# Optimization experiments

Hardware: AMD Instinct MI355X
Metric: run time of the kernel (lower is better)

## Reference

```python
import jax, jax.numpy as jnp
import numpy as np

N, CIN, COUT = 8, 256, 512
HEADS, DK, DV = 8, 256, 256
MAP = 32          # H = W = map_size
KS, PAD = 3, 1
DKH = DK // HEADS  # 32
DVH = DV // HEADS  # 32
CONV_OUT = COUT - DV  # 256


def conv2d(x, w, b, stride=1, padding=0):
    out = jax.lax.conv_general_dilated(
        x, w, (stride, stride), [(padding, padding), (padding, padding)],
        dimension_numbers=("NCHW", "OIHW", "NCHW"))
    return out + b[None, :, None, None]


def rel_to_abs(x):
    # x: [B, G, L, 2L-1] relative logits -> [B, G, L, L] absolute (skewing trick)
    B, G, L, _ = x.shape
    x = jnp.pad(x, ((0, 0), (0, 0), (0, 0), (0, 1)))          # [B,G,L,2L]
    flat = x.reshape(B, G, L * 2 * L)
    flat = jnp.pad(flat, ((0, 0), (0, 0), (0, L - 1)))
    return flat.reshape(B, G, L + 1, 2 * L - 1)[:, :, :L, L - 1:]


def setup_inputs() -> dict:
    key = jax.random.key(0)
    ks = jax.random.split(key, 16)
    def w(k, shape, fan_in):
        return jax.random.normal(k, shape, jnp.float32) * (fan_in ** -0.5)
    inp = {
        "x": jax.random.normal(ks[0], (N, CIN, MAP, MAP), jnp.float32),
        "conv_w": w(ks[1], (CONV_OUT, CIN, KS, KS), CIN * KS * KS),
        "conv_b": jnp.zeros((CONV_OUT,), jnp.float32),
        "q_w": w(ks[2], (DK, CIN, KS, KS), CIN * KS * KS),
        "q_b": jnp.zeros((DK,), jnp.float32),
        "k_w": w(ks[3], (DK, CIN, KS, KS), CIN * KS * KS),
        "k_b": jnp.zeros((DK,), jnp.float32),
        "v_w": w(ks[4], (DV, CIN, KS, KS), CIN * KS * KS),
        "v_b": jnp.zeros((DV,), jnp.float32),
        "attn_w": w(ks[5], (DV, DV, 1, 1), DV),
        "attn_b": jnp.zeros((DV,), jnp.float32),
        "width_mat": jax.random.normal(ks[6], (2 * MAP - 1, DKH), jnp.float32) * (DKH ** -0.5),
        "height_mat": jax.random.normal(ks[7], (2 * MAP - 1, DKH), jnp.float32) * (DKH ** -0.5),
    }
    return inp


def reference(x, conv_w, conv_b, q_w, q_b, k_w, k_b, v_w, v_b,
              attn_w, attn_b, width_mat, height_mat):
    conv_maps = conv2d(x, conv_w, conv_b, 1, PAD)            # [N, 256, H, W]
    H = W = MAP
    q = conv2d(x, q_w, q_b, 1, PAD).reshape(N, HEADS, DKH, H, W)
    k = conv2d(x, k_w, k_b, 1, PAD).reshape(N, HEADS, DKH, H, W)
    v = conv2d(x, v_w, v_b, 1, PAD).reshape(N, HEADS, DVH, H, W)

    qf = q.reshape(N, HEADS, DKH, H * W)
    kf = k.reshape(N, HEADS, DKH, H * W)
    vf = v.reshape(N, HEADS, DVH, H * W)
    logits = jnp.einsum("nhdq,nhdk->nhqk", qf, kf)           # [N,h,HW,HW]

    qp = q.transpose(0, 1, 3, 4, 2)                          # [N,h,H,W,dkh]
    # width relative logits: depends on (hq, wq, wk), broadcast over hk
    rel_w = jnp.einsum("nhyxd,rd->nhyxr", qp, width_mat)     # [N,h,H,W,2W-1]
    abs_w = rel_to_abs(rel_w.reshape(N, HEADS * H, W, 2 * W - 1)
                       ).reshape(N, HEADS, H, W, W)          # [N,h,hq,wq,wk]
    # height relative logits: depends on (wq, hq, hk), broadcast over wk
    rel_h = jnp.einsum("nhyxd,rd->nhxyr", qp, height_mat)    # [N,h,W,H,2H-1]
    abs_h = rel_to_abs(rel_h.reshape(N, HEADS * W, H, 2 * H - 1)
                       ).reshape(N, HEADS, W, H, H)          # [N,h,wq,hq,hk]

    w_bias = abs_w[:, :, :, :, None, :]                      # [N,h,hq,wq,1,wk]
    h_bias = abs_h.transpose(0, 1, 3, 2, 4)[..., None]       # [N,h,hq,wq,hk,1]
    logits = (logits.reshape(N, HEADS, H, W, H, W) + h_bias + w_bias
              ).reshape(N, HEADS, H * W, H * W)
    logits = logits * (DKH ** -0.5)

    weights = jax.nn.softmax(logits, axis=-1)
    attn = jnp.einsum("nhqk,nhdk->nhqd", weights, vf)        # [N,h,HW,dvh]
    # faithful to torch .view quirk: row-major reshape [HW,dvh] -> [dvh,H,W]
    attn_maps = attn.reshape(N, HEADS * DVH, H, W)
    attn_maps = conv2d(attn_maps, attn_w, attn_b, 1, 0)
    return jnp.concatenate([conv_maps, attn_maps], axis=1)
```

## Files before the change

### kernel.cpp

```cpp
#include <hip/hip_runtime.h>
#include <hip/hip_bf16.h>


typedef __attribute__((ext_vector_type(8))) __bf16 bf16x8;
typedef __attribute__((ext_vector_type(4))) float f32x4;
typedef unsigned short u16;
typedef unsigned int u32;
typedef __attribute__((ext_vector_type(8))) u16 u16x8;

#define GLD(gp, lp) __builtin_amdgcn_global_load_lds( \
    (const __attribute__((address_space(1))) u32*)(gp), \
    (__attribute__((address_space(3))) u32*)(lp), 16, 0, 0)

static __device__ __forceinline__ u16 f2bf(float f) {
  u32 u = __builtin_bit_cast(u32, f);
  u += 0x7fffu + ((u >> 16) & 1u);
  return (u16)(u >> 16);
}
static __device__ __forceinline__ float bf2f(u16 h) {
  return __builtin_bit_cast(float, (u32)h << 16);
}

__global__ __launch_bounds__(256) void k_cast_w(
    const float* __restrict__ conv_w, const float* __restrict__ q_w,
    const float* __restrict__ k_w, const float* __restrict__ v_w,
    const float* __restrict__ attn_w, u16* __restrict__ W9, u16* __restrict__ W1) {
  __shared__ float t[2304];
  int row = blockIdx.x;
  const float* src = row < 256 ? conv_w : row < 512 ? q_w : row < 768 ? k_w : v_w;
  const float* sr = src + (row & 255) * 2304;
#pragma unroll
  for (int i = threadIdx.x; i < 2304; i += 256) t[i] = sr[i];
  __syncthreads();
  u16* dr = W9 + row * 2304;
#pragma unroll
  for (int i = threadIdx.x; i < 2304; i += 256) {
    int t9 = i >> 8, c = i & 255;
    dr[i] = f2bf(t[c * 9 + t9]);
  }
  if (row < 256) W1[row * 256 + threadIdx.x] = f2bf(attn_w[row * 256 + threadIdx.x]);
}

__global__ void k_xT(const float* __restrict__ x, u16* __restrict__ xT,
                     u16* __restrict__ zpage) {
  if (blockIdx.x == 0 && threadIdx.x < 512) zpage[threadIdx.x] = 0;
  __shared__ float t[32][33];
  int b = blockIdx.x;
  int sb = b & 31, cb = (b >> 5) & 7, n = b >> 8;
  int s0 = sb << 5, c0 = cb << 5;
  int ls = threadIdx.x & 31, lc = threadIdx.x >> 5;
#pragma unroll
  for (int i = 0; i < 4; ++i) {
    int c = lc + i * 8;
    t[c][ls] = x[(((n << 8) + c0 + c) << 10) + s0 + ls];
  }
  __syncthreads();
#pragma unroll
  for (int i = 0; i < 4; ++i) {
    int s = lc + i * 8;
    xT[(((n << 10) + s0 + s) << 8) + c0 + ls] = f2bf(t[ls][s]);
  }
}

__global__ __launch_bounds__(512) void k_gemm_conv(
    const u16* __restrict__ A, const u16* __restrict__ xT, const u16* __restrict__ zpage,
    float* __restrict__ out,
    u16* __restrict__ qb, u16* __restrict__ kb, u16* __restrict__ vb,
    const float* __restrict__ conv_b, const float* __restrict__ q_b,
    const float* __restrict__ k_b, const float* __restrict__ v_b) {
  __shared__ u16 As[8192], Bs[8192];
  f32x4 acc[4][2] = {};
  const int tid = threadIdx.x;
  const int wave = tid >> 6, lane = tid & 63;
  const int wr = wave >> 2, wc = wave & 3;
  const int lr = lane & 15, lk = lane >> 4;
  const int srow = lane >> 3;
  const int scol = (lane & 7) << 3;
  const int bm = blockIdx.x, bn = blockIdx.y;

  int bn_y[2], bn_x[2], bn_base[2];
#pragma unroll
  for (int i = 0; i < 2; ++i) {
    int seg = i * 8 + wave;
    int col = bn * 128 + seg * 8 + srow;
    int n = col >> 10, s = col & 1023;
    bn_y[i] = s >> 5;
    bn_x[i] = s & 31;
    bn_base[i] = n << 10;
  }

  for (int k0 = 0; k0 < 2304; k0 += 64) {
    int t9 = k0 >> 8;
    int dy = t9 / 3 - 1, dx = t9 - (t9 / 3) * 3 - 1;
    int c0 = k0 & 255;
#pragma unroll
    for (int i = 0; i < 2; ++i) {
      int seg = i * 8 + wave;
      GLD(A + (bm * 128 + seg * 8 + srow) * 2304 + k0 + scol, As + seg * 512);
      int sy = bn_y[i] + dy, sx = bn_x[i] + dx;
      bool ok = ((u32)sy < 32u) && ((u32)sx < 32u);
      const u16* src = ok ? (xT + ((bn_base[i] + (sy << 5) + sx) << 8) + c0 + scol)
                          : (zpage + scol);
      GLD(src, Bs + seg * 512);
    }
    __syncthreads();
#pragma unroll
    for (int kk = 0; kk < 2; ++kk) {
      bf16x8 af[4], bv[2];
#pragma unroll
      for (int m = 0; m < 4; ++m)
        af[m] = *(const bf16x8*)&As[(wr * 64 + m * 16 + lr) * 64 + kk * 32 + lk * 8];
#pragma unroll
      for (int n = 0; n < 2; ++n)
        bv[n] = *(const bf16x8*)&Bs[(wc * 32 + n * 16 + lr) * 64 + kk * 32 + lk * 8];
#pragma unroll
      for (int m = 0; m < 4; ++m)
#pragma unroll
        for (int n = 0; n < 2; ++n)
          acc[m][n] = __builtin_amdgcn_mfma_f32_16x16x32_bf16(af[m], bv[n], acc[m][n], 0, 0, 0);
    }
    __syncthreads();
  }

  const int row0 = bm * 128 + wr * 64 + lk * 4;
  const int col0 = bn * 128 + wc * 32 + lr;
#pragma unroll
  for (int m = 0; m < 4; ++m) {
#pragma unroll
    for (int n = 0; n < 2; ++n) {
      int col = col0 + n * 16;
      int nn = col >> 10, s = col & 1023;
#pragma unroll
      for (int j = 0; j < 4; ++j) {
        int c = row0 + m * 16 + j;
        float v = acc[m][n][j];
        if (c < 256) {
          out[((nn << 9) + c) * 1024 + s] = v + conv_b[c];
        } else if (c < 512) {
          int cc = c - 256;
          qb[((((nn << 3) + (cc >> 5)) << 10) + s) * 32 + (cc & 31)] = f2bf(v + q_b[cc]);
        } else if (c < 768) {
          int cc = c - 512;
          kb[((((nn << 3) + (cc >> 5)) << 10) + s) * 32 + (cc & 31)] = f2bf(v + k_b[cc]);
        } else {
          int cc = c - 768;
          vb[((nn << 8) + cc) * 1024 + s] = f2bf(v + v_b[cc]);
        }
      }
    }
  }
}

__global__ __launch_bounds__(256) void k_bias(const u16* __restrict__ qb,
                                              const float* __restrict__ wm,
                                              const float* __restrict__ hm,
                                              float* __restrict__ Bw, float* __restrict__ Bh) {
  int pos = blockIdx.x * blockDim.x + threadIdx.x;
  int s = pos & 1023;
  int y = s >> 5, xx = s & 31;
  float q[32];
  const u16x8* q8 = (const u16x8*)(qb + pos * 32);
#pragma unroll
  for (int v = 0; v < 4; ++v) {
    u16x8 w = q8[v];
#pragma unroll
    for (int e = 0; e < 8; ++e) q[v * 8 + e] = bf2f(w[e]);
  }
  float* bwo = Bw + pos * 32;
  float* bho = Bh + pos * 32;
#pragma unroll 4
  for (int r = 0; r < 32; ++r) {
    const f32x4* wr = (const f32x4*)(wm + (r - xx + 31) * 32);
    const f32x4* hr = (const f32x4*)(hm + (r - y + 31) * 32);
    float aw = 0.f, ah = 0.f;
#pragma unroll
    for (int i = 0; i < 8; ++i) {
      f32x4 wv = wr[i], hv = hr[i];
#pragma unroll
      for (int e = 0; e < 4; ++e) {
        float qd = q[i * 4 + e];
        aw += qd * wv[e];
        ah += qd * hv[e];
      }
    }
    bwo[r] = aw;
    bho[r] = ah;
  }
}

__global__ __launch_bounds__(256) void k_attn(
    const u16* __restrict__ qb, const u16* __restrict__ kb, const u16* __restrict__ vb,
    const float* __restrict__ Bw, const float* __restrict__ Bh, u16* __restrict__ AMT) {
  __shared__ u16 Pl[4][1024];
  const int wave = threadIdx.x >> 6, lane = threadIdx.x & 63;
  const int task = blockIdx.x * 4 + wave;
  const int nh = task >> 6, qg = task & 63;
  const int n = nh >> 3, h = nh & 7;
  const int qbase = qg << 4;
  const int lr = lane & 15, lg = lane >> 4;

  bf16x8 aq = *(const bf16x8*)&qb[((nh << 10) + qbase + lr) * 32 + lg * 8];

  float Bwr[2][4];
#pragma unroll
  for (int p = 0; p < 2; ++p)
#pragma unroll
    for (int j = 0; j < 4; ++j)
      Bwr[p][j] = Bw[((nh << 10) + qbase + lg * 4 + j) * 32 + p * 16 + lr];

  float mrow[4] = {-1e30f, -1e30f, -1e30f, -1e30f};
  float lrow[4] = {0.f, 0.f, 0.f, 0.f};
  f32x4 o[2] = {};
  u16* pl = Pl[wave];

  for (int kt = 0; kt < 16; ++kt) {
    f32x4 zero = {0.f, 0.f, 0.f, 0.f};
    f32x4 sf_[4];
#pragma unroll
    for (int f = 0; f < 4; ++f) {
      bf16x8 bk = *(const bf16x8*)&kb[((nh << 10) + (kt << 6) + f * 16 + lr) * 32 + lg * 8];
      sf_[f] = __builtin_amdgcn_mfma_f32_16x16x32_bf16(aq, bk, zero, 0, 0, 0);
    }
    float Bhr[2][4];
#pragma unroll
    for (int p = 0; p < 2; ++p)
#pragma unroll
      for (int j = 0; j < 4; ++j)
        Bhr[p][j] = Bh[((nh << 10) + qbase + lg * 4 + j) * 32 + (kt << 1) + p];
    float tv[4][4];
#pragma unroll
    for (int f = 0; f < 4; ++f)
#pragma unroll
      for (int j = 0; j < 4; ++j)
        tv[f][j] = (sf_[f][j] + Bhr[f >> 1][j] + Bwr[f & 1][j]) * 0.17677669529663687f;

    float pv[4][4], sf[4];
#pragma unroll
    for (int j = 0; j < 4; ++j) {
      float vmax = fmaxf(fmaxf(tv[0][j], tv[1][j]), fmaxf(tv[2][j], tv[3][j]));
#pragma unroll
      for (int d = 1; d < 16; d <<= 1) vmax = fmaxf(vmax, __shfl_xor(vmax, d, 64));
      float mn = fmaxf(mrow[j], vmax);
      sf[j] = __expf(mrow[j] - mn);
      mrow[j] = mn;
      float sum = 0.f;
#pragma unroll
      for (int f = 0; f < 4; ++f) {
        float e = __expf(tv[f][j] - mn);
        pv[f][j] = e;
        sum += e;
      }
#pragma unroll
      for (int d = 1; d < 16; d <<= 1) sum += __shfl_xor(sum, d, 64);
      lrow[j] = lrow[j] * sf[j] + sum;
    }
#pragma unroll
    for (int dn = 0; dn < 2; ++dn)
#pragma unroll
      for (int j = 0; j < 4; ++j) o[dn][j] *= sf[j];

#pragma unroll
    for (int f = 0; f < 4; ++f)
#pragma unroll
      for (int j = 0; j < 4; ++j)
        pl[(lg * 4 + j) * 64 + f * 16 + lr] = f2bf(pv[f][j]);
    asm volatile("s_waitcnt lgkmcnt(0)" ::: "memory");
    __builtin_amdgcn_sched_barrier(0);
    bf16x8 pa0 = *(const bf16x8*)&pl[lr * 64 + lg * 8];
    bf16x8 pa1 = *(const bf16x8*)&pl[lr * 64 + 32 + lg * 8];
#pragma unroll
    for (int dn = 0; dn < 2; ++dn) {
      bf16x8 bv0 = *(const bf16x8*)&vb[((n << 8) + (h << 5) + dn * 16 + lr) * 1024 + (kt << 6) + lg * 8];
      o[dn] = __builtin_amdgcn_mfma_f32_16x16x32_bf16(pa0, bv0, o[dn], 0, 0, 0);
      bf16x8 bv1 = *(const bf16x8*)&vb[((n << 8) + (h << 5) + dn * 16 + lr) * 1024 + (kt << 6) + 32 + lg * 8];
      o[dn] = __builtin_amdgcn_mfma_f32_16x16x32_bf16(pa1, bv1, o[dn], 0, 0, 0);
    }
  }
#pragma unroll
  for (int dn = 0; dn < 2; ++dn)
#pragma unroll
    for (int j = 0; j < 4; ++j) {
      int q = qbase + lg * 4 + j;
      int d = dn * 16 + lr;
      float v = o[dn][j] / lrow[j];
      AMT[((n << 10) + ((q & 31) << 5) + d) * 256 + (h << 5) + (q >> 5)] = f2bf(v);
    }
}

static __device__ __forceinline__ void gemm_core(const u16* __restrict__ A,
                                                 const u16* __restrict__ B, int K,
                                                 u16* As, u16* Bs, f32x4 acc[4][4]) {
  const int tid = threadIdx.x;
  const int wave = tid >> 6, lane = tid & 63;
  const int wr = wave >> 1, wc = wave & 1;
  const int lr = lane & 15, lk = lane >> 4;
  const int srow = lane >> 3;
  const int scol = (lane & 7) << 3;
  const int bm = blockIdx.x, bn = blockIdx.y;
  for (int k0 = 0; k0 < K; k0 += 64) {
#pragma unroll
    for (int i = 0; i < 4; ++i) {
      int seg = i * 4 + wave;
      GLD(A + (bm * 128 + seg * 8 + srow) * K + k0 + scol, As + seg * 512);
      GLD(B + (bn * 128 + seg * 8 + srow) * K + k0 + scol, Bs + seg * 512);
    }
    __syncthreads();
#pragma unroll
    for (int kk = 0; kk < 2; ++kk) {
      bf16x8 af[4], bv[4];
#pragma unroll
      for (int m = 0; m < 4; ++m)
        af[m] = *(const bf16x8*)&As[(wr * 64 + m * 16 + lr) * 64 + kk * 32 + lk * 8];
#pragma unroll
      for (int n = 0; n < 4; ++n)
        bv[n] = *(const bf16x8*)&Bs[(wc * 64 + n * 16 + lr) * 64 + kk * 32 + lk * 8];
#pragma unroll
      for (int m = 0; m < 4; ++m)
#pragma unroll
        for (int n = 0; n < 4; ++n)
          acc[m][n] = __builtin_amdgcn_mfma_f32_16x16x32_bf16(af[m], bv[n], acc[m][n], 0, 0, 0);
    }
    __syncthreads();
  }
}

__global__ __launch_bounds__(256) void k_gemm_out(
    const u16* __restrict__ A, const u16* __restrict__ B, float* __restrict__ out,
    const float* __restrict__ attn_b) {
  __shared__ u16 As[8192], Bs[8192];
  f32x4 acc[4][4] = {};
  gemm_core(A, B, 256, As, Bs, acc);
  const int tid = threadIdx.x;
  const int wave = tid >> 6, lane = tid & 63;
  const int wr = wave >> 1, wc = wave & 1;
  const int lr = lane & 15, lk = lane >> 4;
  const int row0 = blockIdx.x * 128 + wr * 64 + lk * 4;
  const int col0 = blockIdx.y * 128 + wc * 64 + lr;
#pragma unroll
  for (int m = 0; m < 4; ++m) {
#pragma unroll
    for (int n = 0; n < 4; ++n) {
      int col = col0 + n * 16;
      int nn = col >> 10, s = col & 1023;
#pragma unroll
      for (int j = 0; j < 4; ++j) {
        int c = row0 + m * 16 + j;
        out[((nn << 9) + 256 + c) * 1024 + s] = acc[m][n][j] + attn_b[c];
      }
    }
  }
}

extern "C" void kernel_launch(void* const* d_in, const int* in_sizes, int n_in,
                              void* d_out, int out_size, void* d_ws, size_t ws_size,
                              hipStream_t stream) {
  const float* x      = (const float*)d_in[0];
  const float* conv_w = (const float*)d_in[1];
  const float* conv_b = (const float*)d_in[2];
  const float* q_w    = (const float*)d_in[3];
  const float* q_b    = (const float*)d_in[4];
  const float* k_w    = (const float*)d_in[5];
  const float* k_b    = (const float*)d_in[6];
  const float* v_w    = (const float*)d_in[7];
  const float* v_b    = (const float*)d_in[8];
  const float* attn_w = (const float*)d_in[9];
  const float* attn_b = (const float*)d_in[10];
  const float* wm     = (const float*)d_in[11];
  const float* hm     = (const float*)d_in[12];
  float* out = (float*)d_out;
  char* ws = (char*)d_ws;

  u16*   W9   = (u16*)(ws + 0);
  u16*   W1   = (u16*)(ws + 4718592);
  u16*   xT   = (u16*)(ws + 4849664);
  u16*   zpg  = (u16*)(ws + 9043968);
  u16*   qbf  = (u16*)(ws + 9044992);
  u16*   kbf  = (u16*)(ws + 13239296);
  u16*   vbf  = (u16*)(ws + 17433600);
  float* Bw   = (float*)(ws + 21627904);
  float* Bh   = (float*)(ws + 30016512);
  u16*   AMT  = (u16*)(ws + 38405120);

  hipLaunchKernelGGL(k_cast_w, dim3(1024), dim3(256), 0, stream,
                     conv_w, q_w, k_w, v_w, attn_w, W9, W1);
  hipLaunchKernelGGL(k_xT, dim3(2048), dim3(256), 0, stream, x, xT, zpg);
  hipLaunchKernelGGL(k_gemm_conv, dim3(8, 64), dim3(512), 0, stream,
                     W9, xT, zpg, out, qbf, kbf, vbf, conv_b, q_b, k_b, v_b);
  hipLaunchKernelGGL(k_bias, dim3(256), dim3(256), 0, stream, qbf, wm, hm, Bw, Bh);
  hipLaunchKernelGGL(k_attn, dim3(1024), dim3(256), 0, stream, qbf, kbf, vbf, Bw, Bh, AMT);
  hipLaunchKernelGGL(k_gemm_out, dim3(2, 64), dim3(256), 0, stream, W1, AMT, out, attn_b);
}
```

Before: 294.3 us.

## Double-buffer conv GEMM with larger 256x128 tiles and swizzled LDS

Restructures the implicit-GEMM convolution kernel to use 256x128 output tiles, so each wave holds a 4x4 MFMA accumulator block and fewer blocks are launched. LDS is double-buffered, with global-to-LDS loads for tile t+2 issued while tile t is computed, gated by a vmcnt wait. An XOR swizzle on LDS columns is meant to avoid bank conflicts, and s_setprio raises wave priority around the MFMA block. This costs more LDS and more registers, which lowers occupancy, and the grid shrinks to 256 blocks.

```diff
diff --git a/kernel.cpp b/kernel.cpp
--- a/kernel.cpp
+++ b/kernel.cpp
@@ -68,66 +68,93 @@
     u16* __restrict__ qb, u16* __restrict__ kb, u16* __restrict__ vb,
     const float* __restrict__ conv_b, const float* __restrict__ q_b,
     const float* __restrict__ k_b, const float* __restrict__ v_b) {
-  __shared__ u16 As[8192], Bs[8192];
-  f32x4 acc[4][2] = {};
+  __shared__ u16 As[2][16384];
+  __shared__ u16 Bs[2][8192];
+  f32x4 acc[4][4] = {};
   const int tid = threadIdx.x;
   const int wave = tid >> 6, lane = tid & 63;
-  const int wr = wave >> 2, wc = wave & 3;
+  const int wr = wave >> 1, wc = wave & 1;
   const int lr = lane & 15, lk = lane >> 4;
   const int srow = lane >> 3;
-  const int scol = (lane & 7) << 3;
+  const int swz = 8 * ((lane & 7) ^ (srow & 7));
   const int bm = blockIdx.x, bn = blockIdx.y;
 
   int bn_y[2], bn_x[2], bn_base[2];
 #pragma unroll
-  for (int i = 0; i < 2; ++i) {
-    int seg = i * 8 + wave;
-    int col = bn * 128 + seg * 8 + srow;
+  for (int r = 0; r < 2; ++r) {
+    int col = bn * 128 + r * 64 + wave * 8 + srow;
     int n = col >> 10, s = col & 1023;
-    bn_y[i] = s >> 5;
-    bn_x[i] = s & 31;
-    bn_base[i] = n << 10;
-  }
-
-  for (int k0 = 0; k0 < 2304; k0 += 64) {
+    bn_y[r] = s >> 5;
+    bn_x[r] = s & 31;
+    bn_base[r] = n << 10;
+  }
+  const u16* a_src[4];
+#pragma unroll
+  for (int a = 0; a < 4; ++a)
+    a_src[a] = A + (bm * 256 + a * 64 + wave * 8 + srow) * 2304 + swz;
+
+  auto stage = [&](int buf, int t) {
+    int k0 = t << 6;
     int t9 = k0 >> 8;
     int dy = t9 / 3 - 1, dx = t9 - (t9 / 3) * 3 - 1;
     int c0 = k0 & 255;
 #pragma unroll
-    for (int i = 0; i < 2; ++i) {
-      int seg = i * 8 + wave;
-      GLD(A + (bm * 128 + seg * 8 + srow) * 2304 + k0 + scol, As + seg * 512);
-      int sy = bn_y[i] + dy, sx = bn_x[i] + dx;
+    for (int a = 0; a < 4; ++a)
+      GLD(a_src[a] + k0, &As[buf][a * 4096 + wave * 512]);
+#pragma unroll
+    for (int r = 0; r < 2; ++r) {
+      int sy = bn_y[r] + dy, sx = bn_x[r] + dx;
       bool ok = ((u32)sy < 32u) && ((u32)sx < 32u);
-      const u16* src = ok ? (xT + ((bn_base[i] + (sy << 5) + sx) << 8) + c0 + scol)
-                          : (zpage + scol);
-      GLD(src, Bs + seg * 512);
-    }
-    __syncthreads();
+      const u16* src = ok ? (xT + ((bn_base[r] + (sy << 5) + sx) << 8) + c0 + swz)
+                          : (zpage + swz);
+      GLD(src, &Bs[buf][r * 4096 + wave * 512]);
+    }
+  };
+
+  const int rswz = lr & 7;
+  const int arow = (wr * 64 + lr) * 64;
+  const int brow = (wc * 64 + lr) * 64;
+
+  auto compute = [&](int buf) {
 #pragma unroll
     for (int kk = 0; kk < 2; ++kk) {
-      bf16x8 af[4], bv[2];
+      const int cswz = (((kk << 2) | lk) ^ rswz) << 3;
+      bf16x8 af[4], bv[4];
 #pragma unroll
       for (int m = 0; m < 4; ++m)
-        af[m] = *(const bf16x8*)&As[(wr * 64 + m * 16 + lr) * 64 + kk * 32 + lk * 8];
-#pragma unroll
-      for (int n = 0; n < 2; ++n)
-        bv[n] = *(const bf16x8*)&Bs[(wc * 32 + n * 16 + lr) * 64 + kk * 32 + lk * 8];
+        af[m] = *(const bf16x8*)&As[buf][arow + m * 1024 + cswz];
+#pragma unroll
+      for (int n = 0; n < 4; ++n)
+        bv[n] = *(const bf16x8*)&Bs[buf][brow + n * 1024 + cswz];
+      __builtin_amdgcn_s_setprio(1);
 #pragma unroll
       for (int m = 0; m < 4; ++m)
 #pragma unroll
-        for (int n = 0; n < 2; ++n)
+        for (int n = 0; n < 4; ++n)
           acc[m][n] = __builtin_amdgcn_mfma_f32_16x16x32_bf16(af[m], bv[n], acc[m][n], 0, 0, 0);
-    }
-    __syncthreads();
-  }
-
-  const int row0 = bm * 128 + wr * 64 + lk * 4;
-  const int col0 = bn * 128 + wc * 32 + lr;
+      __builtin_amdgcn_s_setprio(0);
+    }
+  };
+
+  stage(0, 0);
+  stage(1, 1);
+  for (int t = 0; t < 35; ++t) {
+    asm volatile("s_waitcnt vmcnt(6)" ::: "memory");
+    __builtin_amdgcn_s_barrier();
+    compute(t & 1);
+    __builtin_amdgcn_s_barrier();
+    if (t + 2 < 36) stage(t & 1, t + 2);
+  }
+  asm volatile("s_waitcnt vmcnt(0)" ::: "memory");
+  __builtin_amdgcn_s_barrier();
+  compute(35 & 1);
+
+  const int row0 = bm * 256 + wr * 64 + lk * 4;
+  const int col0 = bn * 128 + wc * 64 + lr;
 #pragma unroll
   for (int m = 0; m < 4; ++m) {
 #pragma unroll
-    for (int n = 0; n < 2; ++n) {
+    for (int n = 0; n < 4; ++n) {
       int col = col0 + n * 16;
       int nn = col >> 10, s = col & 1023;
 #pragma unroll
@@ -384,7 +411,7 @@
   hipLaunchKernelGGL(k_cast_w, dim3(1024), dim3(256), 0, stream,
                      conv_w, q_w, k_w, v_w, attn_w, W9, W1);
   hipLaunchKernelGGL(k_xT, dim3(2048), dim3(256), 0, stream, x, xT, zpg);
-  hipLaunchKernelGGL(k_gemm_conv, dim3(8, 64), dim3(512), 0, stream,
+  hipLaunchKernelGGL(k_gemm_conv, dim3(4, 64), dim3(512), 0, stream,
                      W9, xT, zpg, out, qbf, kbf, vbf, conv_b, q_b, k_b, v_b);
   hipLaunchKernelGGL(k_bias, dim3(256), dim3(256), 0, stream, qbf, wm, hm, Bw, Bh);
   hipLaunchKernelGGL(k_attn, dim3(1024), dim3(256), 0, stream, qbf, kbf, vbf, Bw, Bh, AMT);
```

Measured after the change: 285.9 us. 2.9% less time.
